# Kernel optimization log

Hardware: AMD Instinct MI355X
Metric: run time of the kernel (lower is better)

The kernel has to match this reference:

```python
import jax, jax.numpy as jnp
import numpy as np
import math

B, S, E = 2, 2048, 1024
NH, NKV, HD = 16, 4, 64
GATE_CH = 12

def _rope(x, cos, sin):
    h = x.shape[-1] // 2
    x1, x2 = x[..., :h], x[..., h:]
    return jnp.concatenate((x1 * cos + x2 * sin, x1 * -sin + x2 * cos), axis=-1)

def _rms_norm(x):
    eps = jnp.finfo(x.dtype).eps
    return x * jax.lax.rsqrt(jnp.mean(x * x, axis=-1, keepdims=True) + eps)

def setup_inputs() -> dict:
    key = jax.random.key(0)
    ks = jax.random.split(key, 9)
    x = jax.random.normal(ks[0], (B, S, E), dtype=jnp.float32)
    ve = jax.random.normal(ks[1], (B, S, NKV * HD), dtype=jnp.float32)
    t = jnp.arange(S, dtype=jnp.float32)[:, None]
    inv_freq = 1.0 / (10000.0 ** (jnp.arange(0, HD // 2, dtype=jnp.float32) / (HD // 2)))
    ang = t * inv_freq[None, :]
    cos = jnp.cos(ang)[None, :, None, :]  # (1,S,1,HD//2)
    sin = jnp.sin(ang)[None, :, None, :]
    attn_mask = jnp.tril(jnp.ones((S, S), dtype=bool))[None, None]  # causal (1,1,S,S)
    sc = 0.02
    Wq = jax.random.normal(ks[2], (NH * HD, E), dtype=jnp.float32) * sc
    Wk = jax.random.normal(ks[3], (NKV * HD, E), dtype=jnp.float32) * sc
    Wv = jax.random.normal(ks[4], (NKV * HD, E), dtype=jnp.float32) * sc
    Wproj = jax.random.normal(ks[5], (E, E), dtype=jnp.float32) * sc
    Wgate = jax.random.normal(ks[6], (NKV, GATE_CH), dtype=jnp.float32) * sc
    return {"x": x, "ve": ve, "cos": cos, "sin": sin, "attn_mask": attn_mask,
            "Wq": Wq, "Wk": Wk, "Wv": Wv, "Wproj": Wproj, "Wgate": Wgate}

def reference(x, ve, cos, sin, attn_mask, Wq, Wk, Wv, Wproj, Wgate):
    b, s, _ = x.shape
    q = (x @ Wq.T).reshape(b, s, NH, HD)
    k = (x @ Wk.T).reshape(b, s, NKV, HD)
    v = (x @ Wv.T).reshape(b, s, NKV, HD)
    # value-embedding gating
    gate = 3.0 * jax.nn.sigmoid(x[..., :GATE_CH] @ Wgate.T)  # (b,s,NKV)
    v = v + gate[..., None] * ve.reshape(b, s, NKV, HD)
    # RoPE + QK-RMSNorm
    q = _rms_norm(_rope(q, cos, sin)) * 1.2
    k = _rms_norm(_rope(k, cos, sin)) * 1.2
    # GQA: repeat KV heads
    rep = NH // NKV
    k = jnp.repeat(k, rep, axis=2)
    v = jnp.repeat(v, rep, axis=2)
    q = q.transpose(0, 2, 1, 3)  # (b,h,s,d)
    k = k.transpose(0, 2, 1, 3)
    v = v.transpose(0, 2, 1, 3)
    scores = jnp.einsum('bhqd,bhkd->bhqk', q, k) / math.sqrt(HD)
    scores = jnp.where(attn_mask, scores, jnp.finfo(scores.dtype).min)
    attn = jax.nn.softmax(scores, axis=-1)
    y = jnp.einsum('bhqk,bhkd->bhqd', attn, v)
    y = y.transpose(0, 2, 1, 3).reshape(b, s, NH * HD)
    return y @ Wproj.T
```

## Files before the change

kernel.cpp:

```cpp
#include <hip/hip_runtime.h>
#include <hip/hip_bf16.h>
#include <math.h>

typedef short bf16x8 __attribute__((ext_vector_type(8)));
typedef float f32x4 __attribute__((ext_vector_type(4)));

#define LROW 72
#define NSPLIT 3

__device__ __forceinline__ unsigned short f2bf(float f) {
  union { float f; unsigned int u; } v; v.f = f;
  unsigned int u = v.u;
  unsigned int r = (u + 0x7fffu + ((u >> 16) & 1u)) >> 16;
  return (unsigned short)r;
}
__device__ __forceinline__ float bf2f(unsigned short u) {
  return __uint_as_float((unsigned)u << 16);
}

#if __has_builtin(__builtin_amdgcn_global_load_lds)
#define HAVE_GLD 1
__device__ __forceinline__ void gld16(const void* g, void* l) {
  __builtin_amdgcn_global_load_lds(
      (const __attribute__((address_space(1))) unsigned int*)g,
      (__attribute__((address_space(3))) unsigned int*)l, 16, 0, 0);
}
#else
#define HAVE_GLD 0
#endif

__global__ __launch_bounds__(256) void cvt_all_kernel(const float* __restrict__ x,
                                                      const float* __restrict__ Wq,
                                                      const float* __restrict__ Wk,
                                                      const float* __restrict__ Wv,
                                                      const float* __restrict__ Wproj,
                                                      unsigned short* __restrict__ xb,
                                                      unsigned short* __restrict__ wqkv,
                                                      unsigned short* __restrict__ wpj) {
  int blk = blockIdx.x;
  const float* src;
  unsigned short* dst;
  if (blk < 4096)      { src = x + (size_t)blk * 1024;            dst = xb + (size_t)blk * 1024; }
  else if (blk < 5120) { src = Wq + (size_t)(blk - 4096) * 1024;  dst = wqkv + (size_t)(blk - 4096) * 1024; }
  else if (blk < 5376) { src = Wk + (size_t)(blk - 5120) * 1024;  dst = wqkv + (size_t)(blk - 4096) * 1024; }
  else if (blk < 5632) { src = Wv + (size_t)(blk - 5376) * 1024;  dst = wqkv + (size_t)(blk - 4096) * 1024; }
  else                 { src = Wproj + (size_t)(blk - 5632) * 1024; dst = wpj + (size_t)(blk - 5632) * 1024; }
  int i = threadIdx.x;
  float4 v = ((const float4*)src)[i];
  ushort4 o;
  o.x = f2bf(v.x); o.y = f2bf(v.y); o.z = f2bf(v.z); o.w = f2bf(v.w);
  ((ushort4*)dst)[i] = o;
}

__global__ __launch_bounds__(256) void gemm_qkv_kernel(const unsigned short* __restrict__ A,
                                                       const unsigned short* __restrict__ B,
                                                       const float* __restrict__ ve,
                                                       const float* __restrict__ cosb,
                                                       const float* __restrict__ sinb,
                                                       const float* __restrict__ wgate,
                                                       unsigned short* __restrict__ Q,
                                                       unsigned short* __restrict__ Kd,
                                                       unsigned short* __restrict__ Vt) {
  __shared__ unsigned short As[64 * 64];
  __shared__ unsigned short Bs[128 * 64];
  __shared__ float gLDS[128];
  const int K = 1024;
  int tid = threadIdx.x;
  int wave = tid >> 6, lane = tid & 63, l15 = lane & 15, quad = lane >> 4;
  int wm = (wave >> 1) * 32, wn = (wave & 1) * 64;
  int n0 = blockIdx.x * 128, m0 = blockIdx.y * 64;
  if (n0 >= 1280 && tid < 128) {
    int rl = tid & 63, khl = tid >> 6;
    int kh = ((n0 >> 6) - 20) + khl;
    float dot = 0.f;
#pragma unroll
    for (int jj = 0; jj < 12; jj++)
      dot += bf2f(A[(size_t)(m0 + rl) * 1024 + jj]) * wgate[kh * 12 + jj];
    gLDS[khl * 64 + rl] = 3.0f / (1.0f + __expf(-dot));
  }
  f32x4 acc[2][4];
#pragma unroll
  for (int i = 0; i < 2; i++)
#pragma unroll
    for (int j = 0; j < 4; j++) acc[i][j] = (f32x4){0.f, 0.f, 0.f, 0.f};
  int srow = lane >> 3;
  int scol = ((lane & 7) ^ srow) * 8;
  for (int k0 = 0; k0 < K; k0 += 64) {
    __syncthreads();
#if HAVE_GLD
#pragma unroll
    for (int j = 0; j < 2; j++) {
      int row = wave * 16 + j * 8;
      gld16(A + (size_t)(m0 + row + srow) * K + k0 + scol, As + row * 64 + lane * 8);
    }
#pragma unroll
    for (int j = 0; j < 4; j++) {
      int row = wave * 32 + j * 8;
      gld16(B + (size_t)(n0 + row + srow) * K + k0 + scol, Bs + row * 64 + lane * 8);
    }
#else
#pragma unroll
    for (int j = 0; j < 2; j++) {
      int row = wave * 16 + j * 8;
      *(float4*)(As + row * 64 + lane * 8) = *(const float4*)(A + (size_t)(m0 + row + srow) * K + k0 + scol);
    }
#pragma unroll
    for (int j = 0; j < 4; j++) {
      int row = wave * 32 + j * 8;
      *(float4*)(Bs + row * 64 + lane * 8) = *(const float4*)(B + (size_t)(n0 + row + srow) * K + k0 + scol);
    }
#endif
    __syncthreads();
#pragma unroll
    for (int s = 0; s < 2; s++) {
      bf16x8 af[2], bf[4];
#pragma unroll
      for (int i = 0; i < 2; i++)
        af[i] = *(const bf16x8*)(As + (wm + i * 16 + l15) * 64 + (((s * 4 + quad) ^ (l15 & 7)) * 8));
#pragma unroll
      for (int j = 0; j < 4; j++)
        bf[j] = *(const bf16x8*)(Bs + (wn + j * 16 + l15) * 64 + (((s * 4 + quad) ^ (l15 & 7)) * 8));
#pragma unroll
      for (int i = 0; i < 2; i++)
#pragma unroll
        for (int j = 0; j < 4; j++)
          acc[i][j] = __builtin_amdgcn_mfma_f32_16x16x32_bf16(af[i], bf[j], acc[i][j], 0, 0, 0);
    }
  }
  int hs = (n0 + wn) >> 6;
  if (hs < 20) {
    bool isq = hs < 16;
    float postscale = isq ? 0.216404256f : 1.2f;
#pragma unroll
    for (int i = 0; i < 2; i++) {
#pragma unroll
      for (int r = 0; r < 4; r++) {
        int row = m0 + wm + i * 16 + quad * 4 + r;
        int s = row & 2047, b = row >> 11;
        float c0 = cosb[s * 32 + l15],      s0 = sinb[s * 32 + l15];
        float c1 = cosb[s * 32 + 16 + l15], s1 = sinb[s * 32 + 16 + l15];
        float v0 = acc[i][0][r], v1 = acc[i][1][r], v2 = acc[i][2][r], v3 = acc[i][3][r];
        float n0v = fmaf(v0, c0,  v2 * s0);
        float n1v = fmaf(v1, c1,  v3 * s1);
        float n2v = fmaf(v2, c0, -v0 * s0);
        float n3v = fmaf(v3, c1, -v1 * s1);
        float ss = (n0v * n0v + n1v * n1v) + (n2v * n2v + n3v * n3v);
        ss += __shfl_xor(ss, 1, 64); ss += __shfl_xor(ss, 2, 64);
        ss += __shfl_xor(ss, 4, 64); ss += __shfl_xor(ss, 8, 64);
        float sc = rsqrtf(ss * (1.0f / 64.0f) + 1.1920929e-07f) * postscale;
        unsigned short* dp = isq ? Q + ((size_t)(b * 16 + hs) * 2048 + s) * 64
                                 : Kd + ((size_t)(b * 4 + hs - 16) * 2048 + s) * 64;
        dp[l15]      = f2bf(n0v * sc);
        dp[16 + l15] = f2bf(n1v * sc);
        dp[32 + l15] = f2bf(n2v * sc);
        dp[48 + l15] = f2bf(n3v * sc);
      }
    }
  } else {
    int kh = hs - 20;
#pragma unroll
    for (int i = 0; i < 2; i++) {
#pragma unroll
      for (int r = 0; r < 4; r++) {
        int rl = wm + i * 16 + quad * 4 + r;
        int row = m0 + rl, s = row & 2047, b = row >> 11;
        float g = gLDS[(wave & 1) * 64 + rl];
        const float* vep = ve + (size_t)row * 256 + kh * 64;
        unsigned short* vp = Vt + ((size_t)(b * 4 + kh) * 64) * 2048 + s;
#pragma unroll
        for (int j = 0; j < 4; j++) {
          float vv = fmaf(g, vep[j * 16 + l15], acc[i][j][r]);
          vp[(size_t)(j * 16 + l15) * 2048] = f2bf(vv);
        }
      }
    }
  }
}

__global__ __launch_bounds__(256, 3) void flash_kernel(const unsigned short* __restrict__ Q,
                                                       const unsigned short* __restrict__ K,
                                                       const unsigned short* __restrict__ Vt,
                                                       unsigned short* __restrict__ accP,
                                                       float* __restrict__ lP) {
  __shared__ unsigned short Ks[64 * 64];
  __shared__ unsigned short Vs[64 * 64];
  __shared__ unsigned short Ps[4 * 32 * LROW];
  int pair = blockIdx.x, h = blockIdx.y, bc = blockIdx.z;
  int b = bc / NSPLIT, c = bc % NSPLIT;
  int hb = b * 16 + h;
  int kh = h >> 2;
  int tid = threadIdx.x, wave = tid >> 6, lane = tid & 63, l15 = lane & 15, quad = lane >> 4;
  int l7 = l15 & 7;
  const unsigned short* Kg = K + (size_t)(b * 4 + kh) * 2048 * 64;
  const unsigned short* Vg = Vt + (size_t)(b * 4 + kh) * 64 * 2048;
  unsigned short* Pw = Ps + wave * 32 * LROW;
  int row0 = tid >> 3, col8 = (tid & 7) * 8;
  int dchunk = (((tid & 7) ^ (row0 & 7)) * 8);

#pragma unroll
  for (int half = 0; half < 2; half++) {
    int qt = (half == 0) ? pair : 15 - pair;
    int NT = 2 * qt + 2;
    int c0t = (NT * c) / NSPLIT;
    int c1t = (NT * (c + 1)) / NSPLIT;
    int q0 = qt * 128;
    int qw = q0 + wave * 32;
    const unsigned short* Qp = Q + (((size_t)hb * 2048) + qw + l15) * 64;
    bf16x8 qf[2][2];
    qf[0][0] = *(const bf16x8*)(Qp + quad * 8);
    qf[0][1] = *(const bf16x8*)(Qp + 32 + quad * 8);
    qf[1][0] = *(const bf16x8*)(Qp + 16 * 64 + quad * 8);
    qf[1][1] = *(const bf16x8*)(Qp + 16 * 64 + 32 + quad * 8);
    f32x4 acc[4][2];
#pragma unroll
    for (int i = 0; i < 4; i++) {
      acc[i][0] = (f32x4){0.f, 0.f, 0.f, 0.f};
      acc[i][1] = (f32x4){0.f, 0.f, 0.f, 0.f};
    }
    float ll[2] = {0.f, 0.f};

    if (c1t > c0t) {
      int kf = c0t * 64;
      float4 pk0 = *(const float4*)(Kg + (size_t)(kf + row0) * 64 + col8);
      float4 pk1 = *(const float4*)(Kg + (size_t)(kf + row0 + 32) * 64 + col8);
      float4 pv0 = *(const float4*)(Vg + (size_t)row0 * 2048 + kf + col8);
      float4 pv1 = *(const float4*)(Vg + (size_t)(row0 + 32) * 2048 + kf + col8);

      for (int kt = c0t; kt < c1t; kt++) {
        int k0 = kt * 64;
        __syncthreads();
        *(float4*)(Ks + row0 * 64 + dchunk) = pk0;
        *(float4*)(Ks + (row0 + 32) * 64 + dchunk) = pk1;
        *(float4*)(Vs + row0 * 64 + dchunk) = pv0;
        *(float4*)(Vs + (row0 + 32) * 64 + dchunk) = pv1;
        if (kt + 1 < c1t) {
          int kn = k0 + 64;
          pk0 = *(const float4*)(Kg + (size_t)(kn + row0) * 64 + col8);
          pk1 = *(const float4*)(Kg + (size_t)(kn + row0 + 32) * 64 + col8);
          pv0 = *(const float4*)(Vg + (size_t)row0 * 2048 + kn + col8);
          pv1 = *(const float4*)(Vg + (size_t)(row0 + 32) * 2048 + kn + col8);
        }
        __syncthreads();

        if (k0 <= qw + 31) {
          f32x4 sv[4][2];
#pragma unroll
          for (int mt = 0; mt < 4; mt++) {
            sv[mt][0] = (f32x4){0.f, 0.f, 0.f, 0.f};
            sv[mt][1] = (f32x4){0.f, 0.f, 0.f, 0.f};
          }
          __builtin_amdgcn_s_setprio(1);
#pragma unroll
          for (int mt = 0; mt < 4; mt++) {
            bf16x8 k0f = *(const bf16x8*)(Ks + (mt * 16 + l15) * 64 + ((quad ^ l7) * 8));
            bf16x8 k1f = *(const bf16x8*)(Ks + (mt * 16 + l15) * 64 + (((4 + quad) ^ l7) * 8));
            sv[mt][0] = __builtin_amdgcn_mfma_f32_16x16x32_bf16(k0f, qf[0][0], sv[mt][0], 0, 0, 0);
            sv[mt][0] = __builtin_amdgcn_mfma_f32_16x16x32_bf16(k1f, qf[0][1], sv[mt][0], 0, 0, 0);
            sv[mt][1] = __builtin_amdgcn_mfma_f32_16x16x32_bf16(k0f, qf[1][0], sv[mt][1], 0, 0, 0);
            sv[mt][1] = __builtin_amdgcn_mfma_f32_16x16x32_bf16(k1f, qf[1][1], sv[mt][1], 0, 0, 0);
          }
          __builtin_amdgcn_s_setprio(0);
          if (k0 + 63 > qw) {
#pragma unroll
            for (int f = 0; f < 2; f++) {
              int qg = qw + f * 16 + l15;
#pragma unroll
              for (int mt = 0; mt < 4; mt++) {
                int kg = k0 + mt * 16 + quad * 4;
#pragma unroll
                for (int r = 0; r < 4; r++)
                  if (kg + r > qg) sv[mt][f][r] = -1e30f;
              }
            }
          }
#pragma unroll
          for (int f = 0; f < 2; f++) {
#pragma unroll
            for (int mt = 0; mt < 4; mt++) {
              float p0 = __builtin_amdgcn_exp2f(sv[mt][f][0]);
              float p1 = __builtin_amdgcn_exp2f(sv[mt][f][1]);
              float p2 = __builtin_amdgcn_exp2f(sv[mt][f][2]);
              float p3 = __builtin_amdgcn_exp2f(sv[mt][f][3]);
              ll[f] += (p0 + p1) + (p2 + p3);
              unsigned int lo = __builtin_amdgcn_perm(__float_as_uint(p1), __float_as_uint(p0), 0x07060302u);
              unsigned int hi = __builtin_amdgcn_perm(__float_as_uint(p3), __float_as_uint(p2), 0x07060302u);
              *(uint2*)(Pw + (f * 16 + l15) * LROW + mt * 16 + quad * 4) = make_uint2(lo, hi);
            }
          }
          __builtin_amdgcn_s_setprio(1);
#pragma unroll
          for (int step = 0; step < 2; step++) {
            bf16x8 pa0 = *(const bf16x8*)(Pw + l15 * LROW + step * 32 + quad * 8);
            bf16x8 pa1 = *(const bf16x8*)(Pw + (16 + l15) * LROW + step * 32 + quad * 8);
#pragma unroll
            for (int nt = 0; nt < 4; nt++) {
              bf16x8 vb = *(const bf16x8*)(Vs + (nt * 16 + l15) * 64 + (((step * 4 + quad) ^ l7) * 8));
              acc[nt][0] = __builtin_amdgcn_mfma_f32_16x16x32_bf16(pa0, vb, acc[nt][0], 0, 0, 0);
              acc[nt][1] = __builtin_amdgcn_mfma_f32_16x16x32_bf16(pa1, vb, acc[nt][1], 0, 0, 0);
            }
          }
          __builtin_amdgcn_s_setprio(0);
        }
      }
    }
    ll[0] += __shfl_xor(ll[0], 16, 64);
    ll[0] += __shfl_xor(ll[0], 32, 64);
    ll[1] += __shfl_xor(ll[1], 16, 64);
    ll[1] += __shfl_xor(ll[1], 32, 64);

    size_t slot = (size_t)(c * 32 + hb) * 2048 + qw;
    if (lane < 16) {
      lP[slot + l15] = ll[0];
      lP[slot + 16 + l15] = ll[1];
    }
    unsigned short* aP = accP + slot * 64;
#pragma unroll
    for (int f = 0; f < 2; f++)
#pragma unroll
      for (int r = 0; r < 4; r++)
#pragma unroll
        for (int nt = 0; nt < 4; nt++)
          aP[(size_t)(f * 16 + quad * 4 + r) * 64 + nt * 16 + l15] = f2bf(acc[nt][f][r]);
  }
}

__global__ __launch_bounds__(256) void merge_kernel(const unsigned short* __restrict__ accP,
                                                    const float* __restrict__ lP,
                                                    unsigned short* __restrict__ Y) {
  int t = blockIdx.x * 256 + threadIdx.x;
  int d4 = (t & 15) * 4;
  int q  = (t >> 4) & 2047;
  int hb = t >> 15;
  const size_t CSTR = (size_t)32 * 2048 * 64;
  size_t pi = ((size_t)hb * 2048 + q) * 64 + d4;
  float y0 = 0.f, y1 = 0.f, y2 = 0.f, y3 = 0.f, l = 0.f;
#pragma unroll
  for (int c = 0; c < NSPLIT; c++) {
    ushort4 a = *(const ushort4*)(accP + pi + c * CSTR);
    y0 += bf2f(a.x); y1 += bf2f(a.y); y2 += bf2f(a.z); y3 += bf2f(a.w);
    l += lP[c * 65536 + hb * 2048 + q];
  }
  float inv = 1.f / l;
  ushort4 o;
  o.x = f2bf(y0 * inv); o.y = f2bf(y1 * inv); o.z = f2bf(y2 * inv); o.w = f2bf(y3 * inv);
  int b = hb >> 4, hh = hb & 15;
  *(ushort4*)(Y + ((size_t)(b * 2048 + q) * 1024) + hh * 64 + d4) = o;
}

__global__ __launch_bounds__(256) void gemm_proj_kernel(const unsigned short* __restrict__ A,
                                                        const unsigned short* __restrict__ B,
                                                        float* __restrict__ C) {
  __shared__ unsigned short As[128 * 64];
  __shared__ unsigned short Bs[64 * 64];
  const int K = 1024, N = 1024;
  int tid = threadIdx.x;
  int wave = tid >> 6, lane = tid & 63, l15 = lane & 15, quad = lane >> 4;
  int wm = (wave >> 1) * 64, wn = (wave & 1) * 32;
  int n0 = blockIdx.x * 64, m0 = blockIdx.y * 128;
  f32x4 acc[4][2];
#pragma unroll
  for (int i = 0; i < 4; i++)
#pragma unroll
    for (int j = 0; j < 2; j++) acc[i][j] = (f32x4){0.f, 0.f, 0.f, 0.f};
  int srow = lane >> 3;
  int scol = ((lane & 7) ^ srow) * 8;
  for (int k0 = 0; k0 < K; k0 += 64) {
    __syncthreads();
#if HAVE_GLD
#pragma unroll
    for (int j = 0; j < 4; j++) {
      int row = wave * 32 + j * 8;
      gld16(A + (size_t)(m0 + row + srow) * K + k0 + scol, As + row * 64 + lane * 8);
    }
#pragma unroll
    for (int j = 0; j < 2; j++) {
      int row = wave * 16 + j * 8;
      gld16(B + (size_t)(n0 + row + srow) * K + k0 + scol, Bs + row * 64 + lane * 8);
    }
#else
#pragma unroll
    for (int j = 0; j < 4; j++) {
      int row = wave * 32 + j * 8;
      *(float4*)(As + row * 64 + lane * 8) = *(const float4*)(A + (size_t)(m0 + row + srow) * K + k0 + scol);
    }
#pragma unroll
    for (int j = 0; j < 2; j++) {
      int row = wave * 16 + j * 8;
      *(float4*)(Bs + row * 64 + lane * 8) = *(const float4*)(B + (size_t)(n0 + row + srow) * K + k0 + scol);
    }
#endif
    __syncthreads();
#pragma unroll
    for (int s = 0; s < 2; s++) {
      bf16x8 af[4], bf[2];
#pragma unroll
      for (int i = 0; i < 4; i++)
        af[i] = *(const bf16x8*)(As + (wm + i * 16 + l15) * 64 + (((s * 4 + quad) ^ (l15 & 7)) * 8));
#pragma unroll
      for (int j = 0; j < 2; j++)
        bf[j] = *(const bf16x8*)(Bs + (wn + j * 16 + l15) * 64 + (((s * 4 + quad) ^ (l15 & 7)) * 8));
#pragma unroll
      for (int i = 0; i < 4; i++)
#pragma unroll
        for (int j = 0; j < 2; j++)
          acc[i][j] = __builtin_amdgcn_mfma_f32_16x16x32_bf16(af[i], bf[j], acc[i][j], 0, 0, 0);
    }
  }
#pragma unroll
  for (int i = 0; i < 4; i++)
#pragma unroll
    for (int j = 0; j < 2; j++)
#pragma unroll
      for (int r = 0; r < 4; r++)
        C[(size_t)(m0 + wm + i * 16 + quad * 4 + r) * N + n0 + wn + j * 16 + l15] = acc[i][j][r];
}

extern "C" void kernel_launch(void* const* d_in, const int* in_sizes, int n_in,
                              void* d_out, int out_size, void* d_ws, size_t ws_size,
                              hipStream_t stream) {
  const float* x     = (const float*)d_in[0];
  const float* ve    = (const float*)d_in[1];
  const float* cosb  = (const float*)d_in[2];
  const float* sinb  = (const float*)d_in[3];
  const float* Wq    = (const float*)d_in[5];
  const float* Wk    = (const float*)d_in[6];
  const float* Wv    = (const float*)d_in[7];
  const float* Wproj = (const float*)d_in[8];
  const float* Wgate = (const float*)d_in[9];
  float* out = (float*)d_out;
  char* ws = (char*)d_ws;

  size_t o = 0;
  unsigned short* xb   = (unsigned short*)(ws + o); o += (size_t)4096 * 1024 * 2;
  unsigned short* wqkv = (unsigned short*)(ws + o); o += (size_t)1536 * 1024 * 2;
  unsigned short* wpj  = (unsigned short*)(ws + o); o += (size_t)1024 * 1024 * 2;
  unsigned short* Qb   = (unsigned short*)(ws + o); o += (size_t)2 * 16 * 2048 * 64 * 2;
  unsigned short* Kb   = (unsigned short*)(ws + o); o += (size_t)2 * 4 * 2048 * 64 * 2;
  unsigned short* Vb   = (unsigned short*)(ws + o); o += (size_t)2 * 4 * 2048 * 64 * 2;
  unsigned short* Yb   = (unsigned short*)(ws + o); o += (size_t)4096 * 1024 * 2;
  unsigned short* accP = (unsigned short*)(ws + o); o += (size_t)NSPLIT * 32 * 2048 * 64 * 2;
  float*          lP   = (float*)(ws + o);          o += (size_t)NSPLIT * 32 * 2048 * 4;

  hipLaunchKernelGGL(cvt_all_kernel, dim3(6656), dim3(256), 0, stream,
                     x, Wq, Wk, Wv, Wproj, xb, wqkv, wpj);
  hipLaunchKernelGGL(gemm_qkv_kernel, dim3(12, 64), dim3(256), 0, stream,
                     xb, wqkv, ve, cosb, sinb, Wgate, Qb, Kb, Vb);
  hipLaunchKernelGGL(flash_kernel, dim3(8, 16, 2 * NSPLIT), dim3(256), 0, stream,
                     Qb, Kb, Vb, accP, lP);
  hipLaunchKernelGGL(merge_kernel, dim3(4096), dim3(256), 0, stream, accP, lP, Yb);
  hipLaunchKernelGGL(gemm_proj_kernel, dim3(16, 32), dim3(256), 0, stream, Yb, wpj, out);
}
```

Baseline: 176.0 us.

## Fuse x bf16 conversion into QKV GEMM and double-buffer LDS in both GEMMs

Removes the separate fp32-to-bf16 conversion pass over x. The QKV GEMM now loads fp32 x directly into registers and converts it while staging into LDS, and the gate dot product reads fp32 x. Both GEMMs switch to double-buffered LDS tiles, prefetching the next k-tile while computing the current one, with one barrier per iteration. In exchange, LDS use doubles and fp32 A loads raise register pressure and global traffic per tile, which may lower occupancy.

```diff
diff --git a/kernel.cpp b/kernel.cpp
--- a/kernel.cpp
+++ b/kernel.cpp
@@ -29,22 +29,26 @@
 #define HAVE_GLD 0
 #endif
 
-__global__ __launch_bounds__(256) void cvt_all_kernel(const float* __restrict__ x,
-                                                      const float* __restrict__ Wq,
-                                                      const float* __restrict__ Wk,
-                                                      const float* __restrict__ Wv,
-                                                      const float* __restrict__ Wproj,
-                                                      unsigned short* __restrict__ xb,
-                                                      unsigned short* __restrict__ wqkv,
-                                                      unsigned short* __restrict__ wpj) {
+__device__ __forceinline__ void st_bf8(unsigned short* d, float4 lo, float4 hi) {
+  union { unsigned short s[8]; bf16x8 v; } u;
+  u.s[0] = f2bf(lo.x); u.s[1] = f2bf(lo.y); u.s[2] = f2bf(lo.z); u.s[3] = f2bf(lo.w);
+  u.s[4] = f2bf(hi.x); u.s[5] = f2bf(hi.y); u.s[6] = f2bf(hi.z); u.s[7] = f2bf(hi.w);
+  *(bf16x8*)d = u.v;
+}
+
+__global__ __launch_bounds__(256) void cvt_w_kernel(const float* __restrict__ Wq,
+                                                    const float* __restrict__ Wk,
+                                                    const float* __restrict__ Wv,
+                                                    const float* __restrict__ Wproj,
+                                                    unsigned short* __restrict__ wqkv,
+                                                    unsigned short* __restrict__ wpj) {
   int blk = blockIdx.x;
   const float* src;
   unsigned short* dst;
-  if (blk < 4096)      { src = x + (size_t)blk * 1024;            dst = xb + (size_t)blk * 1024; }
-  else if (blk < 5120) { src = Wq + (size_t)(blk - 4096) * 1024;  dst = wqkv + (size_t)(blk - 4096) * 1024; }
-  else if (blk < 5376) { src = Wk + (size_t)(blk - 5120) * 1024;  dst = wqkv + (size_t)(blk - 4096) * 1024; }
-  else if (blk < 5632) { src = Wv + (size_t)(blk - 5376) * 1024;  dst = wqkv + (size_t)(blk - 4096) * 1024; }
-  else                 { src = Wproj + (size_t)(blk - 5632) * 1024; dst = wpj + (size_t)(blk - 5632) * 1024; }
+  if (blk < 1024)      { src = Wq + (size_t)blk * 1024;            dst = wqkv + (size_t)blk * 1024; }
+  else if (blk < 1280) { src = Wk + (size_t)(blk - 1024) * 1024;   dst = wqkv + (size_t)blk * 1024; }
+  else if (blk < 1536) { src = Wv + (size_t)(blk - 1280) * 1024;   dst = wqkv + (size_t)blk * 1024; }
+  else                 { src = Wproj + (size_t)(blk - 1536) * 1024; dst = wpj + (size_t)(blk - 1536) * 1024; }
   int i = threadIdx.x;
   float4 v = ((const float4*)src)[i];
   ushort4 o;
@@ -52,17 +56,17 @@
   ((ushort4*)dst)[i] = o;
 }
 
-__global__ __launch_bounds__(256) void gemm_qkv_kernel(const unsigned short* __restrict__ A,
-                                                       const unsigned short* __restrict__ B,
-                                                       const float* __restrict__ ve,
-                                                       const float* __restrict__ cosb,
-                                                       const float* __restrict__ sinb,
-                                                       const float* __restrict__ wgate,
-                                                       unsigned short* __restrict__ Q,
-                                                       unsigned short* __restrict__ Kd,
-                                                       unsigned short* __restrict__ Vt) {
-  __shared__ unsigned short As[64 * 64];
-  __shared__ unsigned short Bs[128 * 64];
+__global__ __launch_bounds__(256, 3) void gemm_qkv_kernel(const float* __restrict__ X,
+                                                          const unsigned short* __restrict__ B,
+                                                          const float* __restrict__ ve,
+                                                          const float* __restrict__ cosb,
+                                                          const float* __restrict__ sinb,
+                                                          const float* __restrict__ wgate,
+                                                          unsigned short* __restrict__ Q,
+                                                          unsigned short* __restrict__ Kd,
+                                                          unsigned short* __restrict__ Vt) {
+  __shared__ unsigned short As[2][64 * 64];
+  __shared__ unsigned short Bs[2][128 * 64];
   __shared__ float gLDS[128];
   const int K = 1024;
   int tid = threadIdx.x;
@@ -75,7 +79,7 @@
     float dot = 0.f;
 #pragma unroll
     for (int jj = 0; jj < 12; jj++)
-      dot += bf2f(A[(size_t)(m0 + rl) * 1024 + jj]) * wgate[kh * 12 + jj];
+      dot += X[(size_t)(m0 + rl) * 1024 + jj] * wgate[kh * 12 + jj];
     gLDS[khl * 64 + rl] = 3.0f / (1.0f + __expf(-dot));
   }
   f32x4 acc[2][4];
@@ -85,47 +89,76 @@
     for (int j = 0; j < 4; j++) acc[i][j] = (f32x4){0.f, 0.f, 0.f, 0.f};
   int srow = lane >> 3;
   int scol = ((lane & 7) ^ srow) * 8;
+  const float* Ag0 = X + (size_t)(m0 + wave * 16 + srow) * 1024 + scol;
+  const float* Ag1 = Ag0 + (size_t)8 * 1024;
+  int aldst0 = (wave * 16) * 64 + lane * 8;
+  int aldst1 = (wave * 16 + 8) * 64 + lane * 8;
+
+  float4 a0l = *(const float4*)(Ag0);
+  float4 a0h = *(const float4*)(Ag0 + 4);
+  float4 a1l = *(const float4*)(Ag1);
+  float4 a1h = *(const float4*)(Ag1 + 4);
+#if HAVE_GLD
+#pragma unroll
+  for (int j = 0; j < 4; j++) {
+    int row = wave * 32 + j * 8;
+    gld16(B + (size_t)(n0 + row + srow) * K + scol, Bs[0] + row * 64 + lane * 8);
+  }
+#else
+#pragma unroll
+  for (int j = 0; j < 4; j++) {
+    int row = wave * 32 + j * 8;
+    *(float4*)(Bs[0] + row * 64 + lane * 8) = *(const float4*)(B + (size_t)(n0 + row + srow) * K + scol);
+  }
+#endif
+  st_bf8(As[0] + aldst0, a0l, a0h);
+  st_bf8(As[0] + aldst1, a1l, a1h);
+  __syncthreads();
+
   for (int k0 = 0; k0 < K; k0 += 64) {
-    __syncthreads();
+    int cur = (k0 >> 6) & 1;
+    const unsigned short* Ac = As[cur];
+    const unsigned short* Bc = Bs[cur];
+    bool more = (k0 + 64 < K);
+    if (more) {
+      a0l = *(const float4*)(Ag0 + k0 + 64);
+      a0h = *(const float4*)(Ag0 + k0 + 68);
+      a1l = *(const float4*)(Ag1 + k0 + 64);
+      a1h = *(const float4*)(Ag1 + k0 + 68);
 #if HAVE_GLD
 #pragma unroll
-    for (int j = 0; j < 2; j++) {
-      int row = wave * 16 + j * 8;
-      gld16(A + (size_t)(m0 + row + srow) * K + k0 + scol, As + row * 64 + lane * 8);
-    }
-#pragma unroll
-    for (int j = 0; j < 4; j++) {
-      int row = wave * 32 + j * 8;
-      gld16(B + (size_t)(n0 + row + srow) * K + k0 + scol, Bs + row * 64 + lane * 8);
-    }
+      for (int j = 0; j < 4; j++) {
+        int row = wave * 32 + j * 8;
+        gld16(B + (size_t)(n0 + row + srow) * K + k0 + 64 + scol, Bs[cur ^ 1] + row * 64 + lane * 8);
+      }
 #else
 #pragma unroll
-    for (int j = 0; j < 2; j++) {
-      int row = wave * 16 + j * 8;
-      *(float4*)(As + row * 64 + lane * 8) = *(const float4*)(A + (size_t)(m0 + row + srow) * K + k0 + scol);
-    }
-#pragma unroll
-    for (int j = 0; j < 4; j++) {
-      int row = wave * 32 + j * 8;
-      *(float4*)(Bs + row * 64 + lane * 8) = *(const float4*)(B + (size_t)(n0 + row + srow) * K + k0 + scol);
-    }
+      for (int j = 0; j < 4; j++) {
+        int row = wave * 32 + j * 8;
+        *(float4*)(Bs[cur ^ 1] + row * 64 + lane * 8) = *(const float4*)(B + (size_t)(n0 + row + srow) * K + k0 + 64 + scol);
+      }
 #endif
-    __syncthreads();
+    }
 #pragma unroll
     for (int s = 0; s < 2; s++) {
       bf16x8 af[2], bf[4];
 #pragma unroll
       for (int i = 0; i < 2; i++)
-        af[i] = *(const bf16x8*)(As + (wm + i * 16 + l15) * 64 + (((s * 4 + quad) ^ (l15 & 7)) * 8));
+        af[i] = *(const bf16x8*)(Ac + (wm + i * 16 + l15) * 64 + (((s * 4 + quad) ^ (l15 & 7)) * 8));
 #pragma unroll
       for (int j = 0; j < 4; j++)
-        bf[j] = *(const bf16x8*)(Bs + (wn + j * 16 + l15) * 64 + (((s * 4 + quad) ^ (l15 & 7)) * 8));
+        bf[j] = *(const bf16x8*)(Bc + (wn + j * 16 + l15) * 64 + (((s * 4 + quad) ^ (l15 & 7)) * 8));
 #pragma unroll
       for (int i = 0; i < 2; i++)
 #pragma unroll
         for (int j = 0; j < 4; j++)
           acc[i][j] = __builtin_amdgcn_mfma_f32_16x16x32_bf16(af[i], bf[j], acc[i][j], 0, 0, 0);
     }
+    if (more) {
+      st_bf8(As[cur ^ 1] + aldst0, a0l, a0h);
+      st_bf8(As[cur ^ 1] + aldst1, a1l, a1h);
+    }
+    __syncthreads();
   }
   int hs = (n0 + wn) >> 6;
   if (hs < 20) {
@@ -350,8 +383,8 @@
 __global__ __launch_bounds__(256) void gemm_proj_kernel(const unsigned short* __restrict__ A,
                                                         const unsigned short* __restrict__ B,
                                                         float* __restrict__ C) {
-  __shared__ unsigned short As[128 * 64];
-  __shared__ unsigned short Bs[64 * 64];
+  __shared__ unsigned short As[2][128 * 64];
+  __shared__ unsigned short Bs[2][64 * 64];
   const int K = 1024, N = 1024;
   int tid = threadIdx.x;
   int wave = tid >> 6, lane = tid & 63, l15 = lane & 15, quad = lane >> 4;
@@ -364,47 +397,76 @@
     for (int j = 0; j < 2; j++) acc[i][j] = (f32x4){0.f, 0.f, 0.f, 0.f};
   int srow = lane >> 3;
   int scol = ((lane & 7) ^ srow) * 8;
+#if HAVE_GLD
+#pragma unroll
+  for (int j = 0; j < 4; j++) {
+    int row = wave * 32 + j * 8;
+    gld16(A + (size_t)(m0 + row + srow) * K + scol, As[0] + row * 64 + lane * 8);
+  }
+#pragma unroll
+  for (int j = 0; j < 2; j++) {
+    int row = wave * 16 + j * 8;
+    gld16(B + (size_t)(n0 + row + srow) * K + scol, Bs[0] + row * 64 + lane * 8);
+  }
+#else
+#pragma unroll
+  for (int j = 0; j < 4; j++) {
+    int row = wave * 32 + j * 8;
+    *(float4*)(As[0] + row * 64 + lane * 8) = *(const float4*)(A + (size_t)(m0 + row + srow) * K + scol);
+  }
+#pragma unroll
+  for (int j = 0; j < 2; j++) {
+    int row = wave * 16 + j * 8;
+    *(float4*)(Bs[0] + row * 64 + lane * 8) = *(const float4*)(B + (size_t)(n0 + row + srow) * K + scol);
+  }
+#endif
+  __syncthreads();
+
   for (int k0 = 0; k0 < K; k0 += 64) {
-    __syncthreads();
+    int cur = (k0 >> 6) & 1;
+    const unsigned short* Ac = As[cur];
+    const unsigned short* Bc = Bs[cur];
+    if (k0 + 64 < K) {
 #if HAVE_GLD
 #pragma unroll
-    for (int j = 0; j < 4; j++) {
-      int row = wave * 32 + j * 8;
-      gld16(A + (size_t)(m0 + row + srow) * K + k0 + scol, As + row * 64 + lane * 8);
-    }
-#pragma unroll
-    for (int j = 0; j < 2; j++) {
-      int row = wave * 16 + j * 8;
-      gld16(B + (size_t)(n0 + row + srow) * K + k0 + scol, Bs + row * 64 + lane * 8);
-    }
+      for (int j = 0; j < 4; j++) {
+        int row = wave * 32 + j * 8;
+        gld16(A + (size_t)(m0 + row + srow) * K + k0 + 64 + scol, As[cur ^ 1] + row * 64 + lane * 8);
+      }
+#pragma unroll
+      for (int j = 0; j < 2; j++) {
+        int row = wave * 16 + j * 8;
+        gld16(B + (size_t)(n0 + row + srow) * K + k0 + 64 + scol, Bs[cur ^ 1] + row * 64 + lane * 8);
+      }
 #else
 #pragma unroll
-    for (int j = 0; j < 4; j++) {
-      int row = wave * 32 + j * 8;
-      *(float4*)(As + row * 64 + lane * 8) = *(const float4*)(A + (size_t)(m0 + row + srow) * K + k0 + scol);
-    }
-#pragma unroll
-    for (int j = 0; j < 2; j++) {
-      int row = wave * 16 + j * 8;
-      *(float4*)(Bs + row * 64 + lane * 8) = *(const float4*)(B + (size_t)(n0 + row + srow) * K + k0 + scol);
-    }
+      for (int j = 0; j < 4; j++) {
+        int row = wave * 32 + j * 8;
+        *(float4*)(As[cur ^ 1] + row * 64 + lane * 8) = *(const float4*)(A + (size_t)(m0 + row + srow) * K + k0 + 64 + scol);
+      }
+#pragma unroll
+      for (int j = 0; j < 2; j++) {
+        int row = wave * 16 + j * 8;
+        *(float4*)(Bs[cur ^ 1] + row * 64 + lane * 8) = *(const float4*)(B + (size_t)(n0 + row + srow) * K + k0 + 64 + scol);
+      }
 #endif
-    __syncthreads();
+    }
 #pragma unroll
     for (int s = 0; s < 2; s++) {
       bf16x8 af[4], bf[2];
 #pragma unroll
       for (int i = 0; i < 4; i++)
-        af[i] = *(const bf16x8*)(As + (wm + i * 16 + l15) * 64 + (((s * 4 + quad) ^ (l15 & 7)) * 8));
+        af[i] = *(const bf16x8*)(Ac + (wm + i * 16 + l15) * 64 + (((s * 4 + quad) ^ (l15 & 7)) * 8));
 #pragma unroll
       for (int j = 0; j < 2; j++)
-        bf[j] = *(const bf16x8*)(Bs + (wn + j * 16 + l15) * 64 + (((s * 4 + quad) ^ (l15 & 7)) * 8));
+        bf[j] = *(const bf16x8*)(Bc + (wn + j * 16 + l15) * 64 + (((s * 4 + quad) ^ (l15 & 7)) * 8));
 #pragma unroll
       for (int i = 0; i < 4; i++)
 #pragma unroll
         for (int j = 0; j < 2; j++)
           acc[i][j] = __builtin_amdgcn_mfma_f32_16x16x32_bf16(af[i], bf[j], acc[i][j], 0, 0, 0);
     }
+    __syncthreads();
   }
 #pragma unroll
   for (int i = 0; i < 4; i++)
@@ -431,7 +493,6 @@
   char* ws = (char*)d_ws;
 
   size_t o = 0;
-  unsigned short* xb   = (unsigned short*)(ws + o); o += (size_t)4096 * 1024 * 2;
   unsigned short* wqkv = (unsigned short*)(ws + o); o += (size_t)1536 * 1024 * 2;
   unsigned short* wpj  = (unsigned short*)(ws + o); o += (size_t)1024 * 1024 * 2;
   unsigned short* Qb   = (unsigned short*)(ws + o); o += (size_t)2 * 16 * 2048 * 64 * 2;
@@ -441,10 +502,10 @@
   unsigned short* accP = (unsigned short*)(ws + o); o += (size_t)NSPLIT * 32 * 2048 * 64 * 2;
   float*          lP   = (float*)(ws + o);          o += (size_t)NSPLIT * 32 * 2048 * 4;
 
-  hipLaunchKernelGGL(cvt_all_kernel, dim3(6656), dim3(256), 0, stream,
-                     x, Wq, Wk, Wv, Wproj, xb, wqkv, wpj);
+  hipLaunchKernelGGL(cvt_w_kernel, dim3(2560), dim3(256), 0, stream,
+                     Wq, Wk, Wv, Wproj, wqkv, wpj);
   hipLaunchKernelGGL(gemm_qkv_kernel, dim3(12, 64), dim3(256), 0, stream,
-                     xb, wqkv, ve, cosb, sinb, Wgate, Qb, Kb, Vb);
+                     x, wqkv, ve, cosb, sinb, Wgate, Qb, Kb, Vb);
   hipLaunchKernelGGL(flash_kernel, dim3(8, 16, 2 * NSPLIT), dim3(256), 0, stream,
                      Qb, Kb, Vb, accP, lP);
   hipLaunchKernelGGL(merge_kernel, dim3(4096), dim3(256), 0, stream, accP, lP, Yb);
```

Result: slower. 183.4 us (+4.2%).
